# Kernel tuning notes

Hardware: AMD Instinct MI355X
Metric: run time of the kernel (lower is better)

Reference implementation:

```python
import jax, jax.numpy as jnp
import numpy as np

D_K = 64

def setup_inputs() -> dict:
    key = jax.random.key(0)
    ks = jax.random.split(key, 5)
    B, H, N, Dk, Dv = 32, 16, 512, 64, 64
    Q = jax.random.normal(ks[0], (B, H, N, Dk), dtype=jnp.float32)
    K = jax.random.normal(ks[1], (B, H, N, Dk), dtype=jnp.float32)
    V = jax.random.normal(ks[2], (B, H, N, Dv), dtype=jnp.float32)
    pos_ids = jnp.arange(H * N, dtype=jnp.int64 if jax.config.jax_enable_x64 else jnp.int32).reshape(1, H, N)
    pos_k_table = jax.random.normal(ks[3], (H * N, Dk), dtype=jnp.float32)
    pos_v_table = jax.random.normal(ks[4], (H * N, Dv), dtype=jnp.float32)
    return {"Q": Q, "K": K, "V": V, "pos_ids": pos_ids,
            "pos_k_table": pos_k_table, "pos_v_table": pos_v_table}

def reference(Q, K, V, pos_ids, pos_k_table, pos_v_table):
    # Positional embedding lookup: [1, H, N, Dk] / [1, H, N, Dv]
    K_pos = pos_k_table[pos_ids]
    V_pos = pos_v_table[pos_ids]
    scale = 1.0 / np.sqrt(D_K).astype(np.float32)
    # scores: [B, H, Nq, Nk]
    scores = jnp.einsum('bhqd,bhkd->bhqk', Q, K + K_pos) * scale
    attn = jax.nn.softmax(scores, axis=-1)
    context = jnp.einsum('bhqk,bhkd->bhqd', attn, V + V_pos)
    return (context, attn)
```

## Files before the change

### kernel.cpp

```cpp
#include <hip/hip_runtime.h>
#include <hip/hip_bf16.h>

typedef float fx4 __attribute__((ext_vector_type(4)));
typedef __bf16 bf16x8 __attribute__((ext_vector_type(8)));

#define NN 512
#define ND 64
#define NH 16
#define NB 32
#define BH (NB * NH)

__global__ __launch_bounds__(256)
void prep_kernel(const float* __restrict__ K, const float* __restrict__ V,
                 const int* __restrict__ pos_ids,
                 const float* __restrict__ pkt, const float* __restrict__ pvt,
                 __bf16* __restrict__ Kb, __bf16* __restrict__ VT)
{
    __shared__ alignas(16) __bf16 vt[64][72];
    const int bid = blockIdx.x;
    const int bh = bid >> 3, nc = bid & 7;
    const int h  = bh & (NH - 1);
    const int t  = threadIdx.x;
    const int nl = t >> 2;
    const int dq = (t & 3) * 16;
    const int n  = nc * 64 + nl;
    const int pid = pos_ids[h * NN + n];
    const size_t rowb = (size_t)(bh * NN + n) * ND;

    {
        const float* kr = K + rowb + dq;
        const float* pr = pkt + (size_t)pid * ND + dq;
        bf16x8 o[2];
#pragma unroll
        for (int q = 0; q < 4; ++q) {
            fx4 a = *(const fx4*)(kr + q * 4);
            fx4 b = *(const fx4*)(pr + q * 4);
#pragma unroll
            for (int i = 0; i < 4; ++i) o[q >> 1][(q & 1) * 4 + i] = (__bf16)(a[i] + b[i]);
        }
        *(bf16x8*)(Kb + rowb + dq)     = o[0];
        *(bf16x8*)(Kb + rowb + dq + 8) = o[1];
    }
    {
        const float* vr = V + rowb + dq;
        const float* pr = pvt + (size_t)pid * ND + dq;
        bf16x8 o[2];
#pragma unroll
        for (int q = 0; q < 4; ++q) {
            fx4 a = *(const fx4*)(vr + q * 4);
            fx4 b = *(const fx4*)(pr + q * 4);
#pragma unroll
            for (int i = 0; i < 4; ++i) o[q >> 1][(q & 1) * 4 + i] = (__bf16)(a[i] + b[i]);
        }
        *(bf16x8*)&vt[nl][dq]     = o[0];
        *(bf16x8*)&vt[nl][dq + 8] = o[1];
    }
    __syncthreads();
    {
        const int d  = t >> 2;
        const int j0 = (t & 3) * 16;
        bf16x8 o[2];
#pragma unroll
        for (int i = 0; i < 16; ++i) o[i >> 3][i & 7] = vt[j0 + i][d];
        __bf16* dst = VT + ((size_t)bh * ND + d) * NN + nc * 64 + j0;
        *(bf16x8*)dst       = o[0];
        *(bf16x8*)(dst + 8) = o[1];
    }
}

__global__ __launch_bounds__(256, 2)
void attn_main(const float* __restrict__ Q,
               const __bf16* __restrict__ Kb,
               const __bf16* __restrict__ VT,
               float* __restrict__ ctx_out,
               float* __restrict__ attn_out)
{
    const int bid = blockIdx.x;
    const int swz = (bid & 7) * 512 + (bid >> 3);
    const int bh  = swz >> 3;
    const int qb  = swz & 7;
    const int tid = threadIdx.x;
    const int lane = tid & 63, g = lane >> 4, lr = lane & 15;
    const int q0  = qb * 64 + (tid >> 6) * 16;
    const size_t kbase = (size_t)bh * NN * ND;
    const float CEXP = 0.125f * 1.44269504088896340736f;

    bf16x8 qf[2];
#pragma unroll
    for (int ks = 0; ks < 2; ++ks) {
        const float* qp = Q + kbase + (size_t)(q0 + lr) * ND + ks * 32 + g * 8;
        fx4 a = *(const fx4*)qp;
        fx4 b = *(const fx4*)(qp + 4);
#pragma unroll
        for (int i = 0; i < 4; ++i) { qf[ks][i] = (__bf16)a[i]; qf[ks][4 + i] = (__bf16)b[i]; }
    }

    fx4 acc[32];
    const fx4 vzero = {0.f, 0.f, 0.f, 0.f};
#pragma unroll
    for (int ct = 0; ct < 32; ++ct) acc[ct] = vzero;

    const __bf16* kp0 = Kb + kbase + (size_t)lr * ND + g * 8;
#pragma unroll
    for (int ct = 0; ct < 32; ++ct) {
        bf16x8 b0 = *(const bf16x8*)(kp0 + (size_t)ct * 16 * ND);
        bf16x8 b1 = *(const bf16x8*)(kp0 + (size_t)ct * 16 * ND + 32);
        acc[ct] = __builtin_amdgcn_mfma_f32_16x16x32_bf16(qf[0], b0, acc[ct], 0, 0, 0);
        acc[ct] = __builtin_amdgcn_mfma_f32_16x16x32_bf16(qf[1], b1, acc[ct], 0, 0, 0);
    }

    float rs[4];
#pragma unroll
    for (int r = 0; r < 4; ++r) {
        float s = 0.f;
#pragma unroll
        for (int ct = 0; ct < 32; ++ct) {
            float p = exp2f(acc[ct][r] * CEXP);
            acc[ct][r] = p;
            s += p;
        }
        s += __shfl_xor(s, 1); s += __shfl_xor(s, 2);
        s += __shfl_xor(s, 4); s += __shfl_xor(s, 8);
        rs[r] = 1.0f / s;
    }

#pragma unroll
    for (int r = 0; r < 4; ++r) {
        float* ap = attn_out + ((size_t)bh * NN + q0 + g * 4 + r) * NN + lr;
#pragma unroll
        for (int ct = 0; ct < 32; ++ct)
            ap[ct * 16] = acc[ct][r] * rs[r];
    }

    asm volatile("s_waitcnt vmcnt(0)" ::: "memory");

    fx4 accp[4];
#pragma unroll
    for (int c = 0; c < 4; ++c) accp[c] = vzero;
    const float* prow = attn_out + ((size_t)bh * NN + q0 + lr) * NN + g * 8;
    const __bf16* vp  = VT + (size_t)bh * ND * NN + (size_t)lr * NN + g * 8;
#pragma unroll
    for (int ks2 = 0; ks2 < 16; ++ks2) {
        fx4 a0 = *(const volatile fx4*)(prow + ks2 * 32);
        fx4 a1 = *(const volatile fx4*)(prow + ks2 * 32 + 4);
        bf16x8 pa;
#pragma unroll
        for (int i = 0; i < 4; ++i) { pa[i] = (__bf16)a0[i]; pa[4 + i] = (__bf16)a1[i]; }
#pragma unroll
        for (int ctd = 0; ctd < 4; ++ctd) {
            bf16x8 vb = *(const bf16x8*)(vp + (size_t)ctd * 16 * NN + ks2 * 32);
            accp[ctd] = __builtin_amdgcn_mfma_f32_16x16x32_bf16(pa, vb, accp[ctd], 0, 0, 0);
        }
    }

#pragma unroll
    for (int ctd = 0; ctd < 4; ++ctd)
#pragma unroll
        for (int r = 0; r < 4; ++r)
            ctx_out[((size_t)bh * NN + q0 + g * 4 + r) * ND + ctd * 16 + lr] = accp[ctd][r];
}

extern "C" void kernel_launch(void* const* d_in, const int* in_sizes, int n_in,
                              void* d_out, int out_size, void* d_ws, size_t ws_size,
                              hipStream_t stream) {
    const float* Q   = (const float*)d_in[0];
    const float* K   = (const float*)d_in[1];
    const float* V   = (const float*)d_in[2];
    const int*   pid = (const int*)d_in[3];
    const float* pkt = (const float*)d_in[4];
    const float* pvt = (const float*)d_in[5];
    float* ctx  = (float*)d_out;
    float* attn = ctx + (size_t)BH * NN * ND;

    __bf16* Kb = (__bf16*)d_ws;
    __bf16* VT = Kb + (size_t)BH * NN * ND;

    hipLaunchKernelGGL(prep_kernel, dim3(BH * 8), dim3(256), 0, stream,
                       K, V, pid, pkt, pvt, Kb, VT);
    hipLaunchKernelGGL(attn_main, dim3(BH * 8), dim3(256), 0, stream,
                       Q, Kb, VT, ctx, attn);
}
```

Before: 1.104 ms.

## Recompute QK scores in two passes and stage probabilities through LDS

The attention kernel drops its 32 register-resident score tiles. A first pass computes QK^T only to accumulate the softmax row sums. A second pass recomputes the scores in chunks of 128 keys, writes unnormalized bf16 probabilities to per-wave LDS, emits normalized coalesced float4 attn stores from LDS, and feeds the PV MFMAs from LDS instead of re-reading attn_out from global memory. Lower register pressure allows raising launch bounds to 4 blocks per SM. In exchange the QK matmul and exp are computed twice, and the stored attn values now pass through bf16 rounding before normalization.

```diff
diff --git a/kernel.cpp b/kernel.cpp
--- a/kernel.cpp
+++ b/kernel.cpp
@@ -68,22 +68,28 @@
     }
 }
 
-__global__ __launch_bounds__(256, 2)
+__global__ __launch_bounds__(256, 4)
 void attn_main(const float* __restrict__ Q,
                const __bf16* __restrict__ Kb,
                const __bf16* __restrict__ VT,
                float* __restrict__ ctx_out,
                float* __restrict__ attn_out)
 {
+    __shared__ alignas(16) __bf16 Pall[4][16][136];
+    __shared__ float rs_lds[4][16];
+
     const int bid = blockIdx.x;
     const int swz = (bid & 7) * 512 + (bid >> 3);
     const int bh  = swz >> 3;
     const int qb  = swz & 7;
     const int tid = threadIdx.x;
+    const int wid = tid >> 6;
     const int lane = tid & 63, g = lane >> 4, lr = lane & 15;
-    const int q0  = qb * 64 + (tid >> 6) * 16;
+    const int q0  = qb * 64 + wid * 16;
     const size_t kbase = (size_t)bh * NN * ND;
     const float CEXP = 0.125f * 1.44269504088896340736f;
+
+    __bf16 (*Pw)[136] = Pall[wid];
 
     bf16x8 qf[2];
 #pragma unroll
@@ -95,61 +101,74 @@
         for (int i = 0; i < 4; ++i) { qf[ks][i] = (__bf16)a[i]; qf[ks][4 + i] = (__bf16)b[i]; }
     }
 
-    fx4 acc[32];
+    const __bf16* kp0 = Kb + kbase + (size_t)lr * ND + g * 8;
     const fx4 vzero = {0.f, 0.f, 0.f, 0.f};
-#pragma unroll
-    for (int ct = 0; ct < 32; ++ct) acc[ct] = vzero;
-
-    const __bf16* kp0 = Kb + kbase + (size_t)lr * ND + g * 8;
-#pragma unroll
+
+    float s4[4] = {0.f, 0.f, 0.f, 0.f};
+#pragma unroll 4
     for (int ct = 0; ct < 32; ++ct) {
         bf16x8 b0 = *(const bf16x8*)(kp0 + (size_t)ct * 16 * ND);
         bf16x8 b1 = *(const bf16x8*)(kp0 + (size_t)ct * 16 * ND + 32);
-        acc[ct] = __builtin_amdgcn_mfma_f32_16x16x32_bf16(qf[0], b0, acc[ct], 0, 0, 0);
-        acc[ct] = __builtin_amdgcn_mfma_f32_16x16x32_bf16(qf[1], b1, acc[ct], 0, 0, 0);
-    }
-
+        fx4 a = __builtin_amdgcn_mfma_f32_16x16x32_bf16(qf[0], b0, vzero, 0, 0, 0);
+        a = __builtin_amdgcn_mfma_f32_16x16x32_bf16(qf[1], b1, a, 0, 0, 0);
+#pragma unroll
+        for (int r = 0; r < 4; ++r) s4[r] += exp2f(a[r] * CEXP);
+    }
     float rs[4];
 #pragma unroll
     for (int r = 0; r < 4; ++r) {
-        float s = 0.f;
-#pragma unroll
-        for (int ct = 0; ct < 32; ++ct) {
-            float p = exp2f(acc[ct][r] * CEXP);
-            acc[ct][r] = p;
-            s += p;
-        }
+        float s = s4[r];
         s += __shfl_xor(s, 1); s += __shfl_xor(s, 2);
         s += __shfl_xor(s, 4); s += __shfl_xor(s, 8);
         rs[r] = 1.0f / s;
     }
-
-#pragma unroll
-    for (int r = 0; r < 4; ++r) {
-        float* ap = attn_out + ((size_t)bh * NN + q0 + g * 4 + r) * NN + lr;
-#pragma unroll
-        for (int ct = 0; ct < 32; ++ct)
-            ap[ct * 16] = acc[ct][r] * rs[r];
-    }
-
-    asm volatile("s_waitcnt vmcnt(0)" ::: "memory");
+    if (lr == 0) {
+#pragma unroll
+        for (int r = 0; r < 4; ++r) rs_lds[wid][g * 4 + r] = rs[r];
+    }
 
     fx4 accp[4];
 #pragma unroll
     for (int c = 0; c < 4; ++c) accp[c] = vzero;
-    const float* prow = attn_out + ((size_t)bh * NN + q0 + lr) * NN + g * 8;
-    const __bf16* vp  = VT + (size_t)bh * ND * NN + (size_t)lr * NN + g * 8;
-#pragma unroll
-    for (int ks2 = 0; ks2 < 16; ++ks2) {
-        fx4 a0 = *(const volatile fx4*)(prow + ks2 * 32);
-        fx4 a1 = *(const volatile fx4*)(prow + ks2 * 32 + 4);
-        bf16x8 pa;
-#pragma unroll
-        for (int i = 0; i < 4; ++i) { pa[i] = (__bf16)a0[i]; pa[4 + i] = (__bf16)a1[i]; }
-#pragma unroll
-        for (int ctd = 0; ctd < 4; ++ctd) {
-            bf16x8 vb = *(const bf16x8*)(vp + (size_t)ctd * 16 * NN + ks2 * 32);
-            accp[ctd] = __builtin_amdgcn_mfma_f32_16x16x32_bf16(pa, vb, accp[ctd], 0, 0, 0);
+
+#pragma unroll
+    for (int ck = 0; ck < 4; ++ck) {
+#pragma unroll
+        for (int ct8 = 0; ct8 < 8; ++ct8) {
+            const int ct = ck * 8 + ct8;
+            bf16x8 b0 = *(const bf16x8*)(kp0 + (size_t)ct * 16 * ND);
+            bf16x8 b1 = *(const bf16x8*)(kp0 + (size_t)ct * 16 * ND + 32);
+            fx4 a = __builtin_amdgcn_mfma_f32_16x16x32_bf16(qf[0], b0, vzero, 0, 0, 0);
+            a = __builtin_amdgcn_mfma_f32_16x16x32_bf16(qf[1], b1, a, 0, 0, 0);
+#pragma unroll
+            for (int r = 0; r < 4; ++r)
+                Pw[g * 4 + r][ct8 * 16 + lr] = (__bf16)exp2f(a[r] * CEXP);
+        }
+
+#pragma unroll
+        for (int i = 0; i < 4; ++i) {
+            const int row  = i * 4 + (lane >> 4);
+            const int colg = (lane & 15) * 8;
+            bf16x8 v = *(const bf16x8*)&Pw[row][colg];
+            const float rsv = rs_lds[wid][row];
+            fx4 o0, o1;
+#pragma unroll
+            for (int j = 0; j < 4; ++j) { o0[j] = (float)v[j] * rsv; o1[j] = (float)v[4 + j] * rsv; }
+            float* ap = attn_out + ((size_t)bh * NN + q0 + row) * NN + ck * 128 + colg;
+            *(fx4*)ap       = o0;
+            *(fx4*)(ap + 4) = o1;
+        }
+
+#pragma unroll
+        for (int k2 = 0; k2 < 4; ++k2) {
+            bf16x8 pa = *(const bf16x8*)&Pw[lr][k2 * 32 + g * 8];
+#pragma unroll
+            for (int ctd = 0; ctd < 4; ++ctd) {
+                const __bf16* vb = VT + ((size_t)bh * ND + ctd * 16 + lr) * NN
+                                 + ck * 128 + k2 * 32 + g * 8;
+                accp[ctd] = __builtin_amdgcn_mfma_f32_16x16x32_bf16(
+                    pa, *(const bf16x8*)vb, accp[ctd], 0, 0, 0);
+            }
         }
     }
 
@@ -157,7 +176,8 @@
     for (int ctd = 0; ctd < 4; ++ctd)
 #pragma unroll
         for (int r = 0; r < 4; ++r)
-            ctx_out[((size_t)bh * NN + q0 + g * 4 + r) * ND + ctd * 16 + lr] = accp[ctd][r];
+            ctx_out[((size_t)bh * NN + q0 + g * 4 + r) * ND + ctd * 16 + lr] =
+                accp[ctd][r] * rs[r];
 }
 
 extern "C" void kernel_launch(void* const* d_in, const int* in_sizes, int n_in,
```

After: 1.050 ms. 1.05x faster.
